# Optimization experiments

Hardware: AMD Instinct MI355X
Metric: run time of the kernel (lower is better)

## Reference

```python
import jax, jax.numpy as jnp
import numpy as np

B, I, H1, H2, E, T = 16384, 512, 256, 128, 8, 2


def setup_inputs() -> dict:
    key = jax.random.key(0)
    ks = jax.random.split(key, 4)
    # Xavier-ish scaling for stability
    x = jax.random.normal(ks[0], (B, I), dtype=jnp.float32)
    W1 = jax.random.normal(ks[1], (E, I, H1), dtype=jnp.float32) / np.sqrt(I)
    b1 = jnp.zeros((E, H1), dtype=jnp.float32)
    W2 = jax.random.normal(ks[2], (E, H1, H2), dtype=jnp.float32) / np.sqrt(H1)
    b2 = jnp.zeros((E, H2), dtype=jnp.float32)
    Wg = jax.random.normal(ks[3], (T, I, E), dtype=jnp.float32) / np.sqrt(I)
    bg = jnp.zeros((T, E), dtype=jnp.float32)
    return {"x": x, "W1": W1, "b1": b1, "W2": W2, "b2": b2, "Wg": Wg, "bg": bg}


def reference(x, W1, b1, W2, b2, Wg, bg):
    # All experts as one grouped GEMM: [E, B, H1]
    h = jax.nn.relu(jnp.einsum('bi,eih->ebh', x, W1) + b1[:, None, :])
    # Last expert layer (lastlayer_reg=True -> act applied): [E, B, H2]
    e_out = jax.nn.relu(jnp.einsum('ebh,eho->ebo', h, W2) + b2[:, None, :])
    # Per-task gates with softmax over experts: [T, B, E]
    gates = jax.nn.softmax(jnp.einsum('bi,tie->tbe', x, Wg) + bg[:, None, :], axis=-1)
    # Gate-weighted combine of expert outputs: [T, B, H2]
    towers = jnp.einsum('tbe,ebo->tbo', gates, e_out)
    return towers
```

## Files before the change

kernel.cpp:

```cpp
#include <hip/hip_runtime.h>
#include <hip/hip_bf16.h>

#define B_  16384
#define I_  512
#define H1_ 256
#define H2_ 128
#define E_  8
#define T_  2

typedef __attribute__((ext_vector_type(8))) short short8;
typedef __attribute__((ext_vector_type(4))) float float4_t;

__device__ inline unsigned short f2bf(float f) {
    union { float f; unsigned u; } v; v.f = f;
    unsigned r = v.u + 0x7FFFu + ((v.u >> 16) & 1u);
    return (unsigned short)(r >> 16);
}

__device__ inline void async_copy16(const unsigned short* g, unsigned short* l) {
    __builtin_amdgcn_global_load_lds(
        (const __attribute__((address_space(1))) void*)g,
        (__attribute__((address_space(3))) void*)l,
        16, 0, 0);
}

__global__ void prep_gates_kernel(const float* __restrict__ x,
                                  unsigned short* __restrict__ xb,
                                  const float* __restrict__ W1,
                                  unsigned short* __restrict__ w1t,
                                  const float* __restrict__ W2,
                                  unsigned short* __restrict__ w2t,
                                  const float* __restrict__ Wg,
                                  const float* __restrict__ bg,
                                  float* __restrict__ gates) {
    __shared__ __align__(16) char smem[16 * 520 * 2 + 4 * 16 * 16 * 4];
    int bid = blockIdx.x;
    int t = threadIdx.x;

    if (bid < 256) {
        unsigned short* wgtL = (unsigned short*)smem;
#pragma unroll
        for (int j = 0; j < 8; ++j) {
            int idx4 = j * 256 + t;
            float4_t wv = ((const float4_t*)Wg)[idx4];
            int e0   = (idx4 & 1) * 4;
            int i    = (idx4 >> 1) & 511;
            int task = idx4 >> 10;
#pragma unroll
            for (int c = 0; c < 4; ++c)
                wgtL[(task * 8 + e0 + c) * 520 + i] = f2bf(wv[c]);
        }
        __syncthreads();

        int w = t >> 6, lane = t & 63;
        int col = lane & 15, quad = lane >> 4;
        int row = bid * 64 + w * 16 + col;
        const float* xr = x + (size_t)row * I_ + quad * 8;
        unsigned short* xw = xb + (size_t)row * I_ + quad * 8;
        const unsigned short* bL = &wgtL[col * 520 + quad * 8];
        float4_t acc = {0.f, 0.f, 0.f, 0.f};
#pragma unroll
        for (int ks = 0; ks < 512; ks += 32) {
            float4_t xa = *(const float4_t*)(xr + ks);
            float4_t xc = *(const float4_t*)(xr + ks + 4);
            short8 a;
            a[0] = (short)f2bf(xa[0]); a[1] = (short)f2bf(xa[1]);
            a[2] = (short)f2bf(xa[2]); a[3] = (short)f2bf(xa[3]);
            a[4] = (short)f2bf(xc[0]); a[5] = (short)f2bf(xc[1]);
            a[6] = (short)f2bf(xc[2]); a[7] = (short)f2bf(xc[3]);
            *(short8*)(xw + ks) = a;
            short8 b = *(const short8*)(bL + ks);
            acc = __builtin_amdgcn_mfma_f32_16x16x32_bf16(a, b, acc, 0, 0, 0);
        }
        float g[4];
#pragma unroll
        for (int p = 0; p < 4; ++p) {
            float v = acc[p] + bg[col];
            float m = v;
            m = fmaxf(m, __shfl_xor(m, 1));
            m = fmaxf(m, __shfl_xor(m, 2));
            m = fmaxf(m, __shfl_xor(m, 4));
            float ev = __expf(v - m);
            float s = ev;
            s += __shfl_xor(s, 1);
            s += __shfl_xor(s, 2);
            s += __shfl_xor(s, 4);
            g[p] = ev / s;
        }
#pragma unroll
        for (int p = 0; p < 4; ++p)
            gates[(size_t)col * B_ + bid * 64 + w * 16 + quad * 4 + p] = g[p];
    } else {
        float (*tile)[33] = (float (*)[33])smem;
        const float* in; unsigned short* outp; int R, C, e, r0, c0;
        if (bid < 1280) {
            int tl = bid - 256;
            e = tl >> 7; int rem = tl & 127;
            R = I_; C = H1_;
            r0 = (rem >> 3) * 32; c0 = (rem & 7) * 32;
            in = W1; outp = w1t;
        } else {
            int tl = bid - 1280;
            e = tl >> 5; int rem = tl & 31;
            R = H1_; C = H2_;
            r0 = (rem >> 2) * 32; c0 = (rem & 3) * 32;
            in = W2; outp = w2t;
        }
        const float* inp = in + (size_t)e * R * C;
        unsigned short* op = outp + (size_t)e * R * C;
        int tx = t & 31, ty = t >> 5;
#pragma unroll
        for (int j = 0; j < 32; j += 8)
            tile[ty + j][tx] = inp[(size_t)(r0 + ty + j) * C + c0 + tx];
        __syncthreads();
#pragma unroll
        for (int j = 0; j < 32; j += 8)
            op[(size_t)(c0 + ty + j) * R + r0 + tx] = f2bf(tile[tx][ty + j]);
    }
}

__global__ void gemm_relu_kernel(const unsigned short* __restrict__ A, size_t aSE,
                                 const unsigned short* __restrict__ Bt, size_t bSE,
                                 const float* __restrict__ bias, int biasSE,
                                 unsigned short* __restrict__ C, size_t cSE,
                                 int K, int lda, int ldb, int ldc) {
    __shared__ unsigned short smem[128 * 136];
    unsigned short* As = smem;
    unsigned short* Bs = smem + 128 * 64;
    int e = blockIdx.z;
    const unsigned short* Ae = A + (size_t)e * aSE;
    const unsigned short* Be = Bt + (size_t)e * bSE;
    const float* biasE = bias + (size_t)e * biasSE;
    unsigned short* Ce = C + (size_t)e * cSE;
    int m0 = blockIdx.x * 128, n0 = blockIdx.y * 128;
    int t = threadIdx.x, w = t >> 6, lane = t & 63;
    int col = lane & 15, quad = lane >> 4;
    int wm = (w & 1) * 64, wn = (w >> 1) * 64;

    float4_t acc[4][4];
#pragma unroll
    for (int mi = 0; mi < 4; ++mi)
#pragma unroll
        for (int ni = 0; ni < 4; ++ni)
            acc[mi][ni] = (float4_t){0.f, 0.f, 0.f, 0.f};

    int rT = t >> 3;
    int gk = (((t & 7) ^ (rT & 7))) * 8;
    const unsigned short* aG = Ae + (size_t)(m0 + rT) * lda + gk;
    const unsigned short* bG = Be + (size_t)(n0 + rT) * ldb + gk;
    unsigned short* aL = As + (size_t)w * 64 * 8;
    unsigned short* bL = Bs + (size_t)w * 64 * 8;

    for (int k0 = 0; k0 < K; k0 += 64) {
#pragma unroll
        for (int j = 0; j < 4; ++j) {
            async_copy16(aG + (size_t)j * 32 * lda + k0, aL + j * 2048);
            async_copy16(bG + (size_t)j * 32 * ldb + k0, bL + j * 2048);
        }
        __syncthreads();
#pragma unroll
        for (int kk = 0; kk < 64; kk += 32) {
            int q = (kk >> 3) + quad;
            short8 af[4], bf[4];
#pragma unroll
            for (int mi = 0; mi < 4; ++mi) {
                int r = wm + mi * 16 + col;
                af[mi] = *(const short8*)&As[r * 64 + ((q ^ (r & 7)) * 8)];
            }
#pragma unroll
            for (int ni = 0; ni < 4; ++ni) {
                int r = wn + ni * 16 + col;
                bf[ni] = *(const short8*)&Bs[r * 64 + ((q ^ (r & 7)) * 8)];
            }
#pragma unroll
            for (int mi = 0; mi < 4; ++mi)
#pragma unroll
                for (int ni = 0; ni < 4; ++ni)
                    acc[mi][ni] = __builtin_amdgcn_mfma_f32_16x16x32_bf16(af[mi], bf[ni], acc[mi][ni], 0, 0, 0);
        }
        __syncthreads();
    }
    unsigned short* Ct = smem;
#pragma unroll
    for (int ni = 0; ni < 4; ++ni) {
        int c = wn + ni * 16 + col;
        float bv = biasE[n0 + c];
#pragma unroll
        for (int mi = 0; mi < 4; ++mi) {
            int rbase = wm + mi * 16 + quad * 4;
#pragma unroll
            for (int p = 0; p < 4; ++p) {
                float v = acc[mi][ni][p] + bv;
                v = v > 0.f ? v : 0.f;
                Ct[(rbase + p) * 136 + c] = f2bf(v);
            }
        }
    }
    __syncthreads();
    int rr = t >> 4, sl = t & 15;
#pragma unroll
    for (int pass = 0; pass < 8; ++pass) {
        int row = pass * 16 + rr;
        short8 vv = *(const short8*)&Ct[row * 136 + sl * 8];
        *(short8*)&Ce[(size_t)(m0 + row) * ldc + n0 + sl * 8] = vv;
    }
}

__global__ __launch_bounds__(512, 4)
void fused_l2_combine_kernel(const unsigned short* __restrict__ h,
                             const unsigned short* __restrict__ w2t,
                             const float* __restrict__ b2,
                             const float* __restrict__ gates,
                             float* __restrict__ out) {
    __shared__ __align__(16) unsigned short ring[36864];
    __shared__ float gL[16][64];

    unsigned short* Aslot = ring;
    unsigned short* Bslot = ring + 12288;

    int b0 = blockIdx.x * 64;
    int t = threadIdx.x, w = t >> 6, lane = t & 63;
    int col = lane & 15, quad = lane >> 4;
    int wm = (w & 1) * 32, wn = (w >> 1) * 32;

    if (t < 256) {
        int te = t >> 4, r4 = (t & 15) * 4;
        *(float4_t*)&gL[te][r4] = *(const float4_t*)&gates[(size_t)te * B_ + b0 + r4];
    }

    int rowA = t >> 3;
    int csw  = ((t & 7) ^ (rowA & 7)) * 8;
    int ldsw = w * 512;

    float4_t tw0[2][2], tw1[2][2];
#pragma unroll
    for (int mi = 0; mi < 2; ++mi)
#pragma unroll
        for (int ni = 0; ni < 2; ++ni) {
            tw0[mi][ni] = (float4_t){0.f, 0.f, 0.f, 0.f};
            tw1[mi][ni] = (float4_t){0.f, 0.f, 0.f, 0.f};
        }

    auto stage = [&](int cid, int slot) {
        int ee = cid >> 2, kc = cid & 3;
        const unsigned short* hE = h + ((size_t)ee * B_ + b0 + rowA) * H1_ + kc * 64 + csw;
        async_copy16(hE, Aslot + slot * 4096 + ldsw);
        const unsigned short* wE = w2t + ((size_t)ee * H2_ + rowA) * H1_ + kc * 64 + csw;
        async_copy16(wE, Bslot + slot * 8192 + ldsw);
        async_copy16(wE + (size_t)64 * H1_, Bslot + slot * 8192 + 4096 + ldsw);
    };

    stage(0, 0);

    float4_t acc[2][2];
    int rd = 0, wr = 1;
#pragma unroll 1
    for (int cid = 0; cid < 32; ++cid) {
        if (cid < 31) {
            stage(cid + 1, wr);
            asm volatile("s_waitcnt vmcnt(3)" ::: "memory");
        } else {
            asm volatile("s_waitcnt vmcnt(0)" ::: "memory");
        }
        asm volatile("s_barrier" ::: "memory");

        if ((cid & 3) == 0) {
#pragma unroll
            for (int mi = 0; mi < 2; ++mi)
#pragma unroll
                for (int ni = 0; ni < 2; ++ni)
                    acc[mi][ni] = (float4_t){0.f, 0.f, 0.f, 0.f};
        }
        const unsigned short* Ac = Aslot + rd * 4096;
        const unsigned short* Bc = Bslot + rd * 8192;
#pragma unroll
        for (int kq = 0; kq < 2; ++kq) {
            int q = kq * 4 + quad;
            short8 af[2], bfv[2];
#pragma unroll
            for (int mi = 0; mi < 2; ++mi) {
                int r = wm + mi * 16 + col;
                af[mi] = *(const short8*)&Ac[r * 64 + ((q ^ (r & 7)) << 3)];
            }
#pragma unroll
            for (int ni = 0; ni < 2; ++ni) {
                int n = wn + ni * 16 + col;
                bfv[ni] = *(const short8*)&Bc[n * 64 + ((q ^ (n & 7)) << 3)];
            }
            __builtin_amdgcn_s_setprio(1);
#pragma unroll
            for (int mi = 0; mi < 2; ++mi)
#pragma unroll
                for (int ni = 0; ni < 2; ++ni)
                    acc[mi][ni] = __builtin_amdgcn_mfma_f32_16x16x32_bf16(
                        af[mi], bfv[ni], acc[mi][ni], 0, 0, 0);
            __builtin_amdgcn_s_setprio(0);
        }

        if ((cid & 3) == 3) {
            int ee = cid >> 2;
#pragma unroll
            for (int ni = 0; ni < 2; ++ni) {
                float bv = b2[ee * H2_ + wn + ni * 16 + col];
#pragma unroll
                for (int mi = 0; mi < 2; ++mi) {
#pragma unroll
                    for (int p = 0; p < 4; ++p) {
                        int rloc = wm + mi * 16 + quad * 4 + p;
                        float v = acc[mi][ni][p] + bv;
                        v = v > 0.f ? v : 0.f;
                        tw0[mi][ni][p] += gL[ee][rloc] * v;
                        tw1[mi][ni][p] += gL[8 + ee][rloc] * v;
                    }
                }
            }
        }
        rd = (rd == 2) ? 0 : rd + 1;
        wr = (wr == 2) ? 0 : wr + 1;
    }

#pragma unroll
    for (int mi = 0; mi < 2; ++mi) {
#pragma unroll
        for (int ni = 0; ni < 2; ++ni) {
            int n = wn + ni * 16 + col;
#pragma unroll
            for (int p = 0; p < 4; ++p) {
                int r = b0 + wm + mi * 16 + quad * 4 + p;
                out[(size_t)r * H2_ + n] = tw0[mi][ni][p];
                out[(size_t)B_ * H2_ + (size_t)r * H2_ + n] = tw1[mi][ni][p];
            }
        }
    }
}

extern "C" void kernel_launch(void* const* d_in, const int* in_sizes, int n_in,
                              void* d_out, int out_size, void* d_ws, size_t ws_size,
                              hipStream_t stream) {
    const float* x  = (const float*)d_in[0];
    const float* W1 = (const float*)d_in[1];
    const float* b1 = (const float*)d_in[2];
    const float* W2 = (const float*)d_in[3];
    const float* b2 = (const float*)d_in[4];
    const float* Wg = (const float*)d_in[5];
    const float* bg = (const float*)d_in[6];
    float* out = (float*)d_out;

    char* ws = (char*)d_ws;
    unsigned short* xb    = (unsigned short*)(ws);
    unsigned short* w1t   = (unsigned short*)(ws + 16777216);
    unsigned short* w2t   = (unsigned short*)(ws + 18874368);
    float*          gates = (float*)(ws + 19398656);
    unsigned short* h     = (unsigned short*)(ws + 20447232);

    prep_gates_kernel<<<dim3(1536), 256, 0, stream>>>(x, xb, W1, w1t, W2, w2t, Wg, bg, gates);

    gemm_relu_kernel<<<dim3(B_ / 128, H1_ / 128, E_), 256, 0, stream>>>(
        xb, 0, w1t, (size_t)H1_ * I_, b1, H1_, h, (size_t)B_ * H1_, I_, I_, I_, H1_);

    fused_l2_combine_kernel<<<dim3(B_ / 64), 512, 0, stream>>>(h, w2t, b2, gates, out);
}
```

Before: 159.0 us.

## Split W2 staging into column halves to shrink LDS ring in combine kernel

The fused layer-2/combine kernel now stages the W2 tile as two 64-column halves in separate iterations, with its own 3-slot ring, while each h tile is reused across two iterations. This cuts the kernel's shared memory from about 72KB to about 48KB per block. The aim is to let more blocks be resident per CU and hide latency better. In exchange the loop runs 64 steps with half the MFMA work per barrier, so synchronization and wait overhead per unit of compute doubles.

```diff
diff --git a/kernel.cpp b/kernel.cpp
--- a/kernel.cpp
+++ b/kernel.cpp
@@ -212,16 +212,15 @@
                              const float* __restrict__ b2,
                              const float* __restrict__ gates,
                              float* __restrict__ out) {
-    __shared__ __align__(16) unsigned short ring[36864];
+    __shared__ __align__(16) unsigned short Aring[3][4096];
+    __shared__ __align__(16) unsigned short Bring[3][4096];
     __shared__ float gL[16][64];
-
-    unsigned short* Aslot = ring;
-    unsigned short* Bslot = ring + 12288;
 
     int b0 = blockIdx.x * 64;
     int t = threadIdx.x, w = t >> 6, lane = t & 63;
     int col = lane & 15, quad = lane >> 4;
-    int wm = (w & 1) * 32, wn = (w >> 1) * 32;
+    int wm = (w & 1) * 32;
+    int wn = (w >> 1) * 16;
 
     if (t < 256) {
         int te = t >> 4, r4 = (t & 15) * 4;
@@ -232,103 +231,112 @@
     int csw  = ((t & 7) ^ (rowA & 7)) * 8;
     int ldsw = w * 512;
 
+    auto stageA = [&](int p) {
+        int ee = p >> 2, kc = p & 3;
+        const unsigned short* hE = h + ((size_t)ee * B_ + b0 + rowA) * H1_ + kc * 64 + csw;
+        async_copy16(hE, &Aring[p % 3][ldsw]);
+    };
+    auto stageB = [&](int cid) {
+        int ee = cid >> 3, kc = (cid >> 1) & 3, nh = cid & 1;
+        const unsigned short* wE = w2t + ((size_t)(ee * H2_ + nh * 64 + rowA)) * H1_ + kc * 64 + csw;
+        async_copy16(wE, &Bring[cid % 3][ldsw]);
+    };
+
     float4_t tw0[2][2], tw1[2][2];
 #pragma unroll
     for (int mi = 0; mi < 2; ++mi)
 #pragma unroll
-        for (int ni = 0; ni < 2; ++ni) {
-            tw0[mi][ni] = (float4_t){0.f, 0.f, 0.f, 0.f};
-            tw1[mi][ni] = (float4_t){0.f, 0.f, 0.f, 0.f};
-        }
-
-    auto stage = [&](int cid, int slot) {
-        int ee = cid >> 2, kc = cid & 3;
-        const unsigned short* hE = h + ((size_t)ee * B_ + b0 + rowA) * H1_ + kc * 64 + csw;
-        async_copy16(hE, Aslot + slot * 4096 + ldsw);
-        const unsigned short* wE = w2t + ((size_t)ee * H2_ + rowA) * H1_ + kc * 64 + csw;
-        async_copy16(wE, Bslot + slot * 8192 + ldsw);
-        async_copy16(wE + (size_t)64 * H1_, Bslot + slot * 8192 + 4096 + ldsw);
-    };
-
-    stage(0, 0);
+        for (int nh = 0; nh < 2; ++nh) {
+            tw0[mi][nh] = (float4_t){0.f, 0.f, 0.f, 0.f};
+            tw1[mi][nh] = (float4_t){0.f, 0.f, 0.f, 0.f};
+        }
+
+    stageA(0);
+    stageB(0);
 
     float4_t acc[2][2];
-    int rd = 0, wr = 1;
+    int lastE = -1;
 #pragma unroll 1
-    for (int cid = 0; cid < 32; ++cid) {
-        if (cid < 31) {
-            stage(cid + 1, wr);
-            asm volatile("s_waitcnt vmcnt(3)" ::: "memory");
+    for (int cid = 0; cid < 64; ++cid) {
+        if ((cid & 1) == 0) {
+            if (cid <= 60) {
+                stageA((cid >> 1) + 1);
+                stageB(cid + 1);
+                asm volatile("s_waitcnt vmcnt(2)" ::: "memory");
+            } else {
+                stageB(63);
+                asm volatile("s_waitcnt vmcnt(1)" ::: "memory");
+            }
         } else {
-            asm volatile("s_waitcnt vmcnt(0)" ::: "memory");
+            if (cid <= 61) {
+                stageB(cid + 1);
+                asm volatile("s_waitcnt vmcnt(1)" ::: "memory");
+            } else {
+                asm volatile("s_waitcnt vmcnt(0)" ::: "memory");
+            }
         }
         asm volatile("s_barrier" ::: "memory");
 
-        if ((cid & 3) == 0) {
+        int ee = cid >> 3, nh = cid & 1;
+        if (ee != lastE) {
+            lastE = ee;
 #pragma unroll
             for (int mi = 0; mi < 2; ++mi)
 #pragma unroll
-                for (int ni = 0; ni < 2; ++ni)
-                    acc[mi][ni] = (float4_t){0.f, 0.f, 0.f, 0.f};
-        }
-        const unsigned short* Ac = Aslot + rd * 4096;
-        const unsigned short* Bc = Bslot + rd * 8192;
+                for (int h2 = 0; h2 < 2; ++h2)
+                    acc[mi][h2] = (float4_t){0.f, 0.f, 0.f, 0.f};
+        }
+
+        const unsigned short* Ac = &Aring[(cid >> 1) % 3][0];
+        const unsigned short* Bc = &Bring[cid % 3][0];
+        int nl = wn + col;
 #pragma unroll
         for (int kq = 0; kq < 2; ++kq) {
             int q = kq * 4 + quad;
-            short8 af[2], bfv[2];
+            short8 af[2], bf;
 #pragma unroll
             for (int mi = 0; mi < 2; ++mi) {
                 int r = wm + mi * 16 + col;
                 af[mi] = *(const short8*)&Ac[r * 64 + ((q ^ (r & 7)) << 3)];
             }
-#pragma unroll
-            for (int ni = 0; ni < 2; ++ni) {
-                int n = wn + ni * 16 + col;
-                bfv[ni] = *(const short8*)&Bc[n * 64 + ((q ^ (n & 7)) << 3)];
-            }
+            bf = *(const short8*)&Bc[nl * 64 + ((q ^ (nl & 7)) << 3)];
             __builtin_amdgcn_s_setprio(1);
 #pragma unroll
             for (int mi = 0; mi < 2; ++mi)
-#pragma unroll
-                for (int ni = 0; ni < 2; ++ni)
-                    acc[mi][ni] = __builtin_amdgcn_mfma_f32_16x16x32_bf16(
-                        af[mi], bfv[ni], acc[mi][ni], 0, 0, 0);
+                acc[mi][nh] = __builtin_amdgcn_mfma_f32_16x16x32_bf16(
+                    af[mi], bf, acc[mi][nh], 0, 0, 0);
             __builtin_amdgcn_s_setprio(0);
         }
 
-        if ((cid & 3) == 3) {
-            int ee = cid >> 2;
-#pragma unroll
-            for (int ni = 0; ni < 2; ++ni) {
-                float bv = b2[ee * H2_ + wn + ni * 16 + col];
+        if ((cid & 7) == 7) {
+#pragma unroll
+            for (int h2 = 0; h2 < 2; ++h2) {
+                float bv = b2[ee * H2_ + h2 * 64 + wn + col];
 #pragma unroll
                 for (int mi = 0; mi < 2; ++mi) {
 #pragma unroll
                     for (int p = 0; p < 4; ++p) {
                         int rloc = wm + mi * 16 + quad * 4 + p;
-                        float v = acc[mi][ni][p] + bv;
+                        float v = acc[mi][h2][p] + bv;
                         v = v > 0.f ? v : 0.f;
-                        tw0[mi][ni][p] += gL[ee][rloc] * v;
-                        tw1[mi][ni][p] += gL[8 + ee][rloc] * v;
+                        tw0[mi][h2][p] += gL[ee][rloc] * v;
+                        tw1[mi][h2][p] += gL[8 + ee][rloc] * v;
                     }
                 }
             }
         }
-        rd = (rd == 2) ? 0 : rd + 1;
-        wr = (wr == 2) ? 0 : wr + 1;
     }
 
 #pragma unroll
     for (int mi = 0; mi < 2; ++mi) {
 #pragma unroll
-        for (int ni = 0; ni < 2; ++ni) {
-            int n = wn + ni * 16 + col;
+        for (int h2 = 0; h2 < 2; ++h2) {
+            int n = h2 * 64 + wn + col;
 #pragma unroll
             for (int p = 0; p < 4; ++p) {
                 int r = b0 + wm + mi * 16 + quad * 4 + p;
-                out[(size_t)r * H2_ + n] = tw0[mi][ni][p];
-                out[(size_t)B_ * H2_ + (size_t)r * H2_ + n] = tw1[mi][ni][p];
+                out[(size_t)r * H2_ + n] = tw0[mi][h2][p];
+                out[(size_t)B_ * H2_ + (size_t)r * H2_ + n] = tw1[mi][h2][p];
             }
         }
     }
```

Result: slower. 176.9 us (+11.3%).
